# Kernel optimization log

Hardware: AMD Instinct MI355X
Metric: run time of the kernel (lower is better)

Reference implementation:

```python
import jax, jax.numpy as jnp
import numpy as np
from itertools import combinations

# ---- G(3,0,1) projective geometric algebra tables (blade order: grades 0..4, lexicographic) ----

def _build_tables():
    blades = [c for g in range(5) for c in combinations(range(4), g)]
    index = {b: i for i, b in enumerate(blades)}
    def mul(a, b, e0_sq):
        lst = list(a) + list(b)
        sign = 1
        for i in range(len(lst)):
            for j in range(len(lst) - 1 - i):
                if lst[j] > lst[j + 1]:
                    lst[j], lst[j + 1] = lst[j + 1], lst[j]
                    sign = -sign
        out, i = [], 0
        while i < len(lst):
            if i + 1 < len(lst) and lst[i] == lst[i + 1]:
                if lst[i] == 0:
                    sign *= e0_sq  # e0^2 = 0 in PGA geometric product
                i += 2
            else:
                out.append(lst[i]); i += 1
        return tuple(out), sign
    GP = np.zeros((16, 16, 16), np.float32)
    WEDGE = np.zeros((16, 16, 16), np.float32)
    for a in blades:
        for b in blades:
            bl, s = mul(a, b, 0)
            if s != 0:
                GP[index[a], index[b], index[bl]] += s
            if not (set(a) & set(b)):
                bl, s = mul(a, b, 1)
                WEDGE[index[a], index[b], index[bl]] += s
    D = np.zeros((16, 16), np.float32)
    for a in blades:
        c = tuple(sorted(set(range(4)) - set(a)))
        bl, s = mul(a, c, 1)  # e_a ^ e_c = s * e0123
        D[index[c], index[a]] = s
    Dinv = np.linalg.inv(D).astype(np.float32)
    # 9 Pin(3,0,1)-equivariant linear basis maps: 5 grade projections + 4 left-mult by e0
    B = np.zeros((9, 16, 16), np.float32)
    for i, a in enumerate(blades):
        B[len(a), i, i] = 1.0
        if 0 not in a:
            tgt = tuple(sorted((0,) + a))
            B[5 + len(a), index[tgt], i] = 1.0
    inner_idx = np.array([i for i, a in enumerate(blades) if 0 not in a])  # invariant inner product skips e0 blades
    return (jnp.asarray(GP), jnp.asarray(WEDGE), jnp.asarray(D), jnp.asarray(Dinv), jnp.asarray(B), jnp.asarray(inner_idx))

GP_T, WEDGE_T, DUAL, DUAL_INV, BASIS, INNER_IDX = _build_tables()
N_HEADS = 8  # gatr SelfAttentionConfig default


def equi_linear(x, W):
    # x: [..., in_ch, 16], W: [out_ch, in_ch, 9] -> [..., out_ch, 16]
    return jnp.einsum('...ik,oib,bjk->...oj', x, W, BASIS)


def equi_norm(x, eps=1e-6):
    sq = jnp.sum(jnp.take(x, INNER_IDX, axis=-1) ** 2, axis=-1)      # [..., C]
    factor = jnp.mean(sq, axis=-1, keepdims=True)[..., None]          # [..., 1, 1]
    return x * jax.lax.rsqrt(factor + eps)


def geometric_product(x, y):
    return jnp.einsum('...i,...j,ijk->...k', x, y, GP_T)


def equi_join(x, y):
    xd = jnp.einsum('ji,...i->...j', DUAL, x)
    yd = jnp.einsum('ji,...i->...j', DUAL, y)
    w = jnp.einsum('...i,...j,ijk->...k', xd, yd, WEDGE_T)
    return jnp.einsum('ji,...i->...j', DUAL_INV, w)


def attention(x, Wq, Wk, Wv, Wo):
    Bb, N, C, _ = x.shape
    ch = C // N_HEADS
    def split(h):
        return h.reshape(Bb, N, N_HEADS, ch, 16).transpose(0, 2, 1, 3, 4)  # [B,H,N,ch,16]
    q = split(equi_linear(x, Wq))
    k = split(equi_linear(x, Wk))
    v = split(equi_linear(x, Wv))
    qi = jnp.take(q, INNER_IDX, axis=-1)
    ki = jnp.take(k, INNER_IDX, axis=-1)
    logits = jnp.einsum('bhnck,bhmck->bhnm', qi, ki) / np.float32(np.sqrt(8 * ch))
    att = jax.nn.softmax(logits, axis=-1)
    out = jnp.einsum('bhnm,bhmck->bhnck', att, v)
    out = out.transpose(0, 2, 1, 3, 4).reshape(Bb, N, C, 16)
    return equi_linear(out, Wo)


def geo_mlp(x, Wl, Wr, Wm):
    C = x.shape[-2]
    half = C // 2
    left = equi_linear(x, Wl)
    right = equi_linear(x, Wr)
    gp = geometric_product(left[..., :half, :], right[..., :half, :])
    jn = equi_join(left[..., half:, :], right[..., half:, :])
    h = jnp.concatenate([gp, jn], axis=-2)
    h = h * jax.nn.gelu(h[..., 0:1], approximate=False)  # scalar-gated GELU
    return equi_linear(h, Wm)


def embed_point(p):
    # PGA point: homogeneous trivector, e123 coefficient 1
    z = jnp.zeros(p.shape[:-1] + (16,), p.dtype)
    z = z.at[..., 11].set(p[..., 2])
    z = z.at[..., 12].set(-p[..., 1])
    z = z.at[..., 13].set(p[..., 0])
    z = z.at[..., 14].set(1.0)
    return z


def reference(points, W_in, Wq, Wk, Wv, Wo, Wl, Wr, Wm, W_out):
    x = embed_point(points)[..., None, :]   # [B, N, 1, 16]
    x = equi_linear(x, W_in)                # [B, N, C, 16]
    def block(xc, p):
        wq, wk, wv, wo, wl, wr, wm = p
        xc = xc + attention(equi_norm(xc), wq, wk, wv, wo)
        xc = xc + geo_mlp(equi_norm(xc), wl, wr, wm)
        return xc, None
    x, _ = jax.lax.scan(block, x, (Wq, Wk, Wv, Wo, Wl, Wr, Wm))
    out = equi_linear(x, W_out)             # [B, N, 1, 16]
    return jnp.mean(out[..., 0], axis=(1, 2))  # [B]


def setup_inputs():
    key = jax.random.key(0)
    ks = jax.random.split(key, 12)
    B, N, C, L = 1, 2048, 16, 10
    def w(k, o, i):
        return jax.random.normal(k, (o, i, 9), jnp.float32) / np.float32(np.sqrt(9.0 * i))
    def wl(k, o, i):
        return jax.random.normal(k, (L, o, i, 9), jnp.float32) / np.float32(np.sqrt(9.0 * i))
    return {
        'points': jax.random.normal(ks[0], (B, N, 3), jnp.float32),
        'W_in': w(ks[1], C, 1),
        'Wq': wl(ks[2], C, C), 'Wk': wl(ks[3], C, C), 'Wv': wl(ks[4], C, C),
        'Wo': wl(ks[5], C, C), 'Wl': wl(ks[6], C, C), 'Wr': wl(ks[7], C, C),
        'Wm': wl(ks[8], C, C), 'W_out': w(ks[9], 1, C),
    }
```

## Files before the change

### kernel.cpp

```cpp
#include <hip/hip_runtime.h>
#include <hip/hip_bf16.h>
#include <math.h>

#define NTOK 2048

typedef short short8v __attribute__((ext_vector_type(8)));
typedef short short4v __attribute__((ext_vector_type(4)));
typedef float f32x4 __attribute__((ext_vector_type(4)));
typedef unsigned u32x4 __attribute__((ext_vector_type(4)));

__device__ __forceinline__ unsigned short f2bf(float x){
  unsigned u = __float_as_uint(x);
  u += 0x7fff + ((u>>16)&1);
  return (unsigned short)(u>>16);
}
__device__ __forceinline__ unsigned pack_bf2(float a, float b){
  __hip_bfloat162 h = __float22bfloat162_rn(float2{a,b});
  return *reinterpret_cast<unsigned*>(&h);
}

struct GEnt { unsigned char i, j, k; signed char s; };

constexpr int IDX2MASK[16] = {0,1,2,4,8,3,5,9,6,10,12,7,11,13,14,15};
constexpr int MASK2IDX[16] = {0,1,2,5,3,6,8,11,4,7,9,12,10,13,14,15};

constexpr int rsign(int a, int b){
  int cnt=0;
  for(int i=0;i<4;++i) if((b>>i)&1) for(int j=i+1;j<4;++j) if((a>>j)&1) cnt++;
  return (cnt&1)?-1:1;
}

struct GPTab { GEnt e[192]; };
constexpr GPTab make_gp(){
  GPTab t{}; int n=0;
  for(int ia=0; ia<16; ++ia) for(int ib=0; ib<16; ++ib){
    int a=IDX2MASK[ia], b=IDX2MASK[ib];
    if(a&b&1) continue;
    t.e[n].i=(unsigned char)ia; t.e[n].j=(unsigned char)ib;
    t.e[n].k=(unsigned char)MASK2IDX[a^b]; t.e[n].s=(signed char)rsign(a,b);
    ++n;
  }
  return t;
}
static constexpr GPTab GP_TAB = make_gp();

struct JTab { GEnt e[81]; };
constexpr JTab make_join(){
  JTab t{}; int n=0;
  for(int ia=0; ia<16; ++ia) for(int ib=0; ib<16; ++ib){
    int a=IDX2MASK[ia], b=IDX2MASK[ib];
    if((a|b)!=15) continue;
    int ca=(~a)&15, cb=(~b)&15, k=a&b, ck=(~k)&15;
    int s = rsign(a,ca)*rsign(b,cb)*rsign(ca,cb)*rsign(k,ck);
    t.e[n].i=(unsigned char)ia; t.e[n].j=(unsigned char)ib;
    t.e[n].k=(unsigned char)MASK2IDX[k]; t.e[n].s=(signed char)s;
    ++n;
  }
  return t;
}
static constexpr JTab J_TAB = make_join();

constexpr int INNER[8] = {0,2,3,4,8,9,10,14};

__device__ __forceinline__ void apply_gp(float* o, const float* a, const float* b){
#pragma unroll
  for(int n=0;n<192;++n){
    const float s = (float)GP_TAB.e[n].s;
    o[GP_TAB.e[n].k] = fmaf(s*a[GP_TAB.e[n].i], b[GP_TAB.e[n].j], o[GP_TAB.e[n].k]);
  }
}
__device__ __forceinline__ void apply_join(float* o, const float* a, const float* b){
#pragma unroll
  for(int n=0;n<81;++n){
    const float s = (float)J_TAB.e[n].s;
    o[J_TAB.e[n].k] = fmaf(s*a[J_TAB.e[n].i], b[J_TAB.e[n].j], o[J_TAB.e[n].k]);
  }
}

__device__ __forceinline__ void elin_row(float acc[16], const float* xin, const float* w0p){
#pragma unroll
  for(int j=0;j<16;++j) acc[j]=0.0f;
#pragma unroll
  for(int i=0;i<16;++i){
    const float* w = w0p + i*9;
    const float4* xp = (const float4*)(xin + i*16);
    float4 A=xp[0], B=xp[1], Cc=xp[2], D=xp[3];
    float w0=w[0],w1=w[1],w2=w[2],w3=w[3],w4=w[4],w5=w[5],w6=w[6],w7=w[7],w8=w[8];
    acc[0] = fmaf(w0, A.x,  acc[0]);
    acc[1] = fmaf(w1, A.y,  acc[1]);
    acc[2] = fmaf(w1, A.z,  acc[2]);
    acc[3] = fmaf(w1, A.w,  acc[3]);
    acc[4] = fmaf(w1, B.x,  acc[4]);
    acc[5] = fmaf(w2, B.y,  acc[5]);
    acc[6] = fmaf(w2, B.z,  acc[6]);
    acc[7] = fmaf(w2, B.w,  acc[7]);
    acc[8] = fmaf(w2, Cc.x, acc[8]);
    acc[9] = fmaf(w2, Cc.y, acc[9]);
    acc[10]= fmaf(w2, Cc.z, acc[10]);
    acc[11]= fmaf(w3, Cc.w, acc[11]);
    acc[12]= fmaf(w3, D.x,  acc[12]);
    acc[13]= fmaf(w3, D.y,  acc[13]);
    acc[14]= fmaf(w3, D.z,  acc[14]);
    acc[15]= fmaf(w4, D.w,  acc[15]);
    acc[1] = fmaf(w5, A.x,  acc[1]);
    acc[5] = fmaf(w6, A.z,  acc[5]);
    acc[6] = fmaf(w6, A.w,  acc[6]);
    acc[7] = fmaf(w6, B.x,  acc[7]);
    acc[11]= fmaf(w7, Cc.x, acc[11]);
    acc[12]= fmaf(w7, Cc.y, acc[12]);
    acc[13]= fmaf(w7, Cc.z, acc[13]);
    acc[15]= fmaf(w8, D.z,  acc[15]);
  }
}

__device__ __forceinline__ float gelu_exact(float x){
  return 0.5f*x*(1.0f+erff(x*0.70710678118654752f));
}

#define WPAD 145
#define TBS  264
#define TPB  8

template<int MODE>
__global__ __launch_bounds__(128) void token_kernel(
    const float* __restrict__ points, const float* __restrict__ Win,
    const float* __restrict__ Wo, const float* __restrict__ Wl,
    const float* __restrict__ Wr, const float* __restrict__ Wm,
    const float* __restrict__ Wq, const float* __restrict__ Wk,
    const float* __restrict__ Wv, const float* __restrict__ Wout,
    const float* __restrict__ ATT, float* __restrict__ X,
    unsigned short* __restrict__ Qg16, unsigned short* __restrict__ Kg16,
    unsigned short* __restrict__ VgT, float* __restrict__ toksum)
{
  __shared__ float wlds[6*16*WPAD];
  __shared__ float buf[TPB*TBS];
  __shared__ float sred[TPB*16];
  const int tid = threadIdx.x;
  const int t = tid>>4, o = tid&15;
  const int n = blockIdx.x*TPB + t;

  auto stage = [&](float* dst, const float* src){
#pragma unroll
    for(int r=0;r<18;++r){
      int k = tid + r*128;
      dst[(k/144)*WPAD + (k%144)] = src[k];
    }
  };
  if (MODE==0){ stage(wlds+3*16*WPAD, Wq); stage(wlds+4*16*WPAD, Wk); stage(wlds+5*16*WPAD, Wv); }
  if (MODE==1){ stage(wlds+0*16*WPAD, Wl); stage(wlds+1*16*WPAD, Wr); stage(wlds+2*16*WPAD, Wm);
                stage(wlds+3*16*WPAD, Wq); stage(wlds+4*16*WPAD, Wk); stage(wlds+5*16*WPAD, Wv); }
  if (MODE==2){ stage(wlds+0*16*WPAD, Wl); stage(wlds+1*16*WPAD, Wr); stage(wlds+2*16*WPAD, Wm); }

  float* tb = buf + t*TBS;
  float xr[16];

  if (MODE==0){
    float px = points[n*3+0], py = points[n*3+1], pz = points[n*3+2];
    float w3 = Win[o*9+3], w8 = Win[o*9+8];
#pragma unroll
    for(int j=0;j<16;++j) xr[j]=0.0f;
    xr[11]= w3*pz; xr[12]= -w3*py; xr[13]= w3*px; xr[14]= w3; xr[15]= w8;
    float4* xg = (float4*)(X + (size_t)n*256 + o*16);
    xg[0]=make_float4(xr[0],xr[1],xr[2],xr[3]);
    xg[1]=make_float4(xr[4],xr[5],xr[6],xr[7]);
    xg[2]=make_float4(xr[8],xr[9],xr[10],xr[11]);
    xg[3]=make_float4(xr[12],xr[13],xr[14],xr[15]);
  } else {
    const float4* xg = (const float4*)(X + (size_t)n*256 + o*16);
    float4 a=xg[0],b=xg[1],c=xg[2],d=xg[3];
    xr[0]=a.x; xr[1]=a.y; xr[2]=a.z; xr[3]=a.w;
    xr[4]=b.x; xr[5]=b.y; xr[6]=b.z; xr[7]=b.w;
    xr[8]=c.x; xr[9]=c.y; xr[10]=c.z; xr[11]=c.w;
    xr[12]=d.x; xr[13]=d.y; xr[14]=d.z; xr[15]=d.w;
    const float4* ag = (const float4*)(ATT + (size_t)n*256 + o*16);
    float4* bp = (float4*)(tb + o*16);
    bp[0]=ag[0]; bp[1]=ag[1]; bp[2]=ag[2]; bp[3]=ag[3];
    __syncthreads();
    float acc[16];
    elin_row(acc, tb, Wo + o*144);
#pragma unroll
    for(int j=0;j<16;++j) xr[j]+=acc[j];
    float s=0;
#pragma unroll
    for(int z=0;z<8;++z){ float v=xr[INNER[z]]; s=fmaf(v,v,s); }
    sred[tid]=s; __syncthreads();
    float tot=0;
#pragma unroll
    for(int c2=0;c2<16;++c2) tot += sred[t*16+c2];
    float f = 1.0f/sqrtf(tot*(1.0f/16.0f)+1e-6f);
    float4* bp2=(float4*)(tb+o*16);
    bp2[0]=make_float4(xr[0]*f,xr[1]*f,xr[2]*f,xr[3]*f);
    bp2[1]=make_float4(xr[4]*f,xr[5]*f,xr[6]*f,xr[7]*f);
    bp2[2]=make_float4(xr[8]*f,xr[9]*f,xr[10]*f,xr[11]*f);
    bp2[3]=make_float4(xr[12]*f,xr[13]*f,xr[14]*f,xr[15]*f);
    __syncthreads();
    float L[16], R[16];
    elin_row(L, tb, wlds+0*16*WPAD + o*WPAD);
    elin_row(R, tb, wlds+1*16*WPAD + o*WPAD);
    float h[16];
#pragma unroll
    for(int j=0;j<16;++j) h[j]=0.0f;
    if (o<8) apply_gp(h,L,R); else apply_join(h,L,R);
    float gel = gelu_exact(h[0]);
#pragma unroll
    for(int j=0;j<16;++j) h[j]*=gel;
    __syncthreads();
    float4* bp3=(float4*)(tb+o*16);
    bp3[0]=make_float4(h[0],h[1],h[2],h[3]);
    bp3[1]=make_float4(h[4],h[5],h[6],h[7]);
    bp3[2]=make_float4(h[8],h[9],h[10],h[11]);
    bp3[3]=make_float4(h[12],h[13],h[14],h[15]);
    __syncthreads();
    float mm2[16];
    elin_row(mm2, tb, wlds+2*16*WPAD + o*WPAD);
#pragma unroll
    for(int j=0;j<16;++j) xr[j]+=mm2[j];
    if (MODE==1){
      float4* xs = (float4*)(X + (size_t)n*256 + o*16);
      xs[0]=make_float4(xr[0],xr[1],xr[2],xr[3]);
      xs[1]=make_float4(xr[4],xr[5],xr[6],xr[7]);
      xs[2]=make_float4(xr[8],xr[9],xr[10],xr[11]);
      xs[3]=make_float4(xr[12],xr[13],xr[14],xr[15]);
    }
  }

  if (MODE==2){
    sred[tid] = Wout[o*9]*xr[0];
    __syncthreads();
    if (o==0){
      float s2=0;
#pragma unroll
      for(int c2=0;c2<16;++c2) s2+=sred[t*16+c2];
      toksum[n]=s2;
    }
    return;
  }

  {
    float s=0;
#pragma unroll
    for(int z=0;z<8;++z){ float v=xr[INNER[z]]; s=fmaf(v,v,s); }
    sred[tid]=s; __syncthreads();
    float tot=0;
#pragma unroll
    for(int c2=0;c2<16;++c2) tot += sred[t*16+c2];
    float f2 = 1.0f/sqrtf(tot*(1.0f/16.0f)+1e-6f);
    float4* bp4=(float4*)(tb+o*16);
    bp4[0]=make_float4(xr[0]*f2,xr[1]*f2,xr[2]*f2,xr[3]*f2);
    bp4[1]=make_float4(xr[4]*f2,xr[5]*f2,xr[6]*f2,xr[7]*f2);
    bp4[2]=make_float4(xr[8]*f2,xr[9]*f2,xr[10]*f2,xr[11]*f2);
    bp4[3]=make_float4(xr[12]*f2,xr[13]*f2,xr[14]*f2,xr[15]*f2);
    __syncthreads();
    float q_[16],k_[16],v_[16];
    elin_row(q_, tb, wlds+3*16*WPAD+o*WPAD);
    elin_row(k_, tb, wlds+4*16*WPAD+o*WPAD);
    elin_row(v_, tb, wlds+5*16*WPAD+o*WPAD);
    int hh=o>>1, cc=o&1;
    {
      unsigned qw[4], kw[4];
#pragma unroll
      for(int j=0;j<4;++j){
        unsigned short a0=f2bf(q_[INNER[2*j]]*0.25f), a1=f2bf(q_[INNER[2*j+1]]*0.25f);
        unsigned short b0=f2bf(k_[INNER[2*j]]),       b1=f2bf(k_[INNER[2*j+1]]);
        qw[j] = (unsigned)a0 | ((unsigned)a1<<16);
        kw[j] = (unsigned)b0 | ((unsigned)b1<<16);
      }
      size_t rb = ((size_t)hh*NTOK + n)*16 + cc*8;
      *(uint4*)(Qg16 + rb) = make_uint4(qw[0],qw[1],qw[2],qw[3]);
      *(uint4*)(Kg16 + rb) = make_uint4(kw[0],kw[1],kw[2],kw[3]);
    }
    __syncthreads();
    {
      float4* vb = (float4*)(tb + o*16);
      vb[0]=make_float4(v_[0],v_[1],v_[2],v_[3]);
      vb[1]=make_float4(v_[4],v_[5],v_[6],v_[7]);
      vb[2]=make_float4(v_[8],v_[9],v_[10],v_[11]);
      vb[3]=make_float4(v_[12],v_[13],v_[14],v_[15]);
    }
    __syncthreads();
#pragma unroll
    for(int pp=0;pp<2;++pp){
      int p  = tid + pp*128;
      int h2 = p>>5, v2 = p&31;
      int oc = 2*h2 + (v2>>4), c2 = v2&15;
      unsigned vw[4];
#pragma unroll
      for(int j=0;j<4;++j){
        unsigned short e0=f2bf(buf[(2*j  )*TBS + oc*16 + c2]);
        unsigned short e1=f2bf(buf[(2*j+1)*TBS + oc*16 + c2]);
        vw[j]=(unsigned)e0 | ((unsigned)e1<<16);
      }
      *(uint4*)(VgT + ((size_t)(h2*32+v2))*NTOK + (size_t)blockIdx.x*TPB) = make_uint4(vw[0],vw[1],vw[2],vw[3]);
    }
  }
}

__global__ __launch_bounds__(512, 8) void attn_kernel(
    const unsigned short* __restrict__ Qg16, const unsigned short* __restrict__ Kg16,
    const unsigned short* __restrict__ VgT,  float* __restrict__ ATT)
{
  __shared__ float cmb[8*32*17];
  __shared__ float ml[8*16*2];
  const int tid = threadIdx.x;
  const int l   = tid & 63, w = tid >> 6;
  const int h   = blockIdx.x >> 7, qb = blockIdx.x & 127;
  const int l15 = l & 15, lg = l >> 4;

  const short4v z4 = {0,0,0,0};
  short8v qf;
  {
    const short4v* qp = (const short4v*)(Qg16 + ((size_t)(h*NTOK + qb*16 + l15))*16 + lg*4);
    qf = __builtin_shufflevector(*qp, z4, 0,1,2,3,4,5,6,7);
  }

  const int key0 = w*256;
  const size_t vrow = ((size_t)(h*32 + l15))*NTOK;

  float mx = -INFINITY;
#pragma unroll 1
  for(int kc=0; kc<256; kc+=64){
#pragma unroll
    for(int t2=0;t2<4;++t2){
      const short4v* kp = (const short4v*)(Kg16 + ((size_t)(h*NTOK + key0 + kc + t2*16 + l15))*16 + lg*4);
      short8v kf = __builtin_shufflevector(*kp, z4, 0,1,2,3,4,5,6,7);
      f32x4 z = {0,0,0,0};
      f32x4 S = __builtin_amdgcn_mfma_f32_16x16x32_bf16(kf, qf, z, 0,0,0);
      mx = fmaxf(mx, fmaxf(fmaxf(S[0],S[1]), fmaxf(S[2],S[3])));
    }
  }
  mx = fmaxf(mx, __shfl_xor(mx, 16));
  mx = fmaxf(mx, __shfl_xor(mx, 32));
  const float M = mx;

  f32x4 acc0 = {0,0,0,0}, acc1 = {0,0,0,0};
  float ls = 0.0f;
#pragma unroll 1
  for(int kc=0; kc<256; kc+=64){
    f32x4 S[4];
#pragma unroll
    for(int t2=0;t2<4;++t2){
      const short4v* kp = (const short4v*)(Kg16 + ((size_t)(h*NTOK + key0 + kc + t2*16 + l15))*16 + lg*4);
      short8v kf = __builtin_shufflevector(*kp, z4, 0,1,2,3,4,5,6,7);
      f32x4 z = {0,0,0,0};
      S[t2] = __builtin_amdgcn_mfma_f32_16x16x32_bf16(kf, qf, z, 0,0,0);
    }
    float p[4][4];
#pragma unroll
    for(int t2=0;t2<4;++t2)
#pragma unroll
      for(int r=0;r<4;++r){ float pv = __expf(S[t2][r]-M); p[t2][r]=pv; ls += pv; }
    u32x4 paw, paw2;
    paw[0]=pack_bf2(p[0][0],p[0][1]); paw[1]=pack_bf2(p[0][2],p[0][3]);
    paw[2]=pack_bf2(p[1][0],p[1][1]); paw[3]=pack_bf2(p[1][2],p[1][3]);
    paw2[0]=pack_bf2(p[2][0],p[2][1]); paw2[1]=pack_bf2(p[2][2],p[2][3]);
    paw2[2]=pack_bf2(p[3][0],p[3][1]); paw2[3]=pack_bf2(p[3][2],p[3][3]);
    short8v pa  = *reinterpret_cast<short8v*>(&paw);
    short8v pa2 = *reinterpret_cast<short8v*>(&paw2);
    size_t vb = vrow + key0 + kc;
    const short4v* v0a = (const short4v*)(VgT + vb + lg*4);
    const short4v* v0b = (const short4v*)(VgT + vb + 16 + lg*4);
    const short4v* v0c = (const short4v*)(VgT + vb + 32 + lg*4);
    const short4v* v0d = (const short4v*)(VgT + vb + 48 + lg*4);
    short8v vb0  = __builtin_shufflevector(*v0a, *v0b, 0,1,2,3,4,5,6,7);
    short8v vb0b = __builtin_shufflevector(*v0c, *v0d, 0,1,2,3,4,5,6,7);
    size_t vb1s = vb + (size_t)16*NTOK;
    const short4v* v1a = (const short4v*)(VgT + vb1s + lg*4);
    const short4v* v1b = (const short4v*)(VgT + vb1s + 16 + lg*4);
    const short4v* v1c = (const short4v*)(VgT + vb1s + 32 + lg*4);
    const short4v* v1d = (const short4v*)(VgT + vb1s + 48 + lg*4);
    short8v vb1  = __builtin_shufflevector(*v1a, *v1b, 0,1,2,3,4,5,6,7);
    short8v vb1b = __builtin_shufflevector(*v1c, *v1d, 0,1,2,3,4,5,6,7);
    acc0 = __builtin_amdgcn_mfma_f32_16x16x32_bf16(pa,  vb0,  acc0, 0,0,0);
    acc0 = __builtin_amdgcn_mfma_f32_16x16x32_bf16(pa2, vb0b, acc0, 0,0,0);
    acc1 = __builtin_amdgcn_mfma_f32_16x16x32_bf16(pa,  vb1,  acc1, 0,0,0);
    acc1 = __builtin_amdgcn_mfma_f32_16x16x32_bf16(pa2, vb1b, acc1, 0,0,0);
  }
  ls += __shfl_xor(ls, 16);
  ls += __shfl_xor(ls, 32);

  {
    float* cw = cmb + w*544;
#pragma unroll
    for(int r=0;r<4;++r){
      cw[ l15     *17 + lg*4 + r] = acc0[r];
      cw[(l15+16) *17 + lg*4 + r] = acc1[r];
    }
    if (lg == 0){
      ml[(w*16 + l15)*2]   = M;
      ml[(w*16 + l15)*2+1] = ls;
    }
  }
  __syncthreads();
  {
    int q = tid & 15, v = tid >> 4;
    float Mg = -INFINITY;
#pragma unroll
    for(int w2=0; w2<8; ++w2) Mg = fmaxf(Mg, ml[(w2*16+q)*2]);
    float L=0, a=0;
#pragma unroll
    for(int w2=0; w2<8; ++w2){
      float ww = __expf(ml[(w2*16+q)*2] - Mg);
      L = fmaf(ml[(w2*16+q)*2+1], ww, L);
      a = fmaf(cmb[w2*544 + v*17 + q], ww, a);
    }
    int n = qb*16 + q;
    ATT[(size_t)n*256 + (size_t)(2*h + (v>>4))*16 + (v&15)] = a/L;
  }
}

__global__ __launch_bounds__(256) void reduce_kernel(const float* __restrict__ tok, float* __restrict__ out){
  int tid=threadIdx.x;
  float s=0;
  for(int i=tid;i<NTOK;i+=256) s+=tok[i];
#pragma unroll
  for(int off=32;off>0;off>>=1) s += __shfl_down(s,off);
  __shared__ float red[4];
  if((tid&63)==0) red[tid>>6]=s;
  __syncthreads();
  if(tid==0) out[0]=(red[0]+red[1]+red[2]+red[3])*(1.0f/2048.0f);
}

extern "C" void kernel_launch(void* const* d_in, const int* in_sizes, int n_in,
                              void* d_out, int out_size, void* d_ws, size_t ws_size,
                              hipStream_t stream){
  const float* points=(const float*)d_in[0];
  const float* Win=(const float*)d_in[1];
  const float* Wq=(const float*)d_in[2];
  const float* Wk=(const float*)d_in[3];
  const float* Wv=(const float*)d_in[4];
  const float* Wo=(const float*)d_in[5];
  const float* Wl=(const float*)d_in[6];
  const float* Wr=(const float*)d_in[7];
  const float* Wm=(const float*)d_in[8];
  const float* Wout=(const float*)d_in[9];
  float* ws=(float*)d_ws;
  float* X    = ws;
  float* ATT  = ws + 524288;
  unsigned short* Qg16 = (unsigned short*)(ws + 1048576);
  unsigned short* Kg16 = (unsigned short*)(ws + 1179648);
  unsigned short* VgT  = (unsigned short*)(ws + 1310720);
  float* tok  = ws + 1572864;
  float* out=(float*)d_out;

  token_kernel<0><<<256,128,0,stream>>>(points,Win,nullptr,nullptr,nullptr,nullptr,
                                        Wq,Wk,Wv,nullptr,nullptr,X,Qg16,Kg16,VgT,nullptr);
  for(int l=0;l<10;++l){
    attn_kernel<<<1024,512,0,stream>>>(Qg16,Kg16,VgT,ATT);
    if(l<9){
      token_kernel<1><<<256,128,0,stream>>>(nullptr,nullptr,
          Wo+l*2304,Wl+l*2304,Wr+l*2304,Wm+l*2304,
          Wq+(l+1)*2304,Wk+(l+1)*2304,Wv+(l+1)*2304,nullptr,
          ATT,X,Qg16,Kg16,VgT,nullptr);
    } else {
      token_kernel<2><<<256,128,0,stream>>>(nullptr,nullptr,
          Wo+l*2304,Wl+l*2304,Wr+l*2304,Wm+l*2304,
          nullptr,nullptr,nullptr,Wout,
          ATT,X,nullptr,nullptr,nullptr,tok);
    }
  }
  reduce_kernel<<<1,256,0,stream>>>(tok,out);
}
```

Before: 677.4 us.

## Split token kernel per-token work across a wavefront with shuffle reductions

Each token is now handled by one 64-lane wavefront instead of 16 threads. The 16 input channels of every equivariant linear layer are split into four partial sums, which are combined with cross-lane shuffles. Weights are re-laid out in LDS as padded 12-float rows so they can be read with vector loads, and Wo is also staged in LDS. Block barriers are replaced by in-wave LDS waits, and the norm and output reductions use shuffles instead of shared memory. The intent is more parallelism and fewer block-wide barriers in the serial token stage. In exchange, each block now re-stages the QKV weights a second time, and lanes that do not write stay idle.

```diff
diff --git a/kernel.cpp b/kernel.cpp
--- a/kernel.cpp
+++ b/kernel.cpp
@@ -77,15 +77,25 @@
   }
 }
 
-__device__ __forceinline__ void elin_row(float acc[16], const float* xin, const float* w0p){
+__device__ __forceinline__ float gelu_exact(float x){
+  return 0.5f*x*(1.0f+erff(x*0.70710678118654752f));
+}
+
+#define TBS 264
+
+__device__ __forceinline__ void elin_part(float acc[16], const float* xin, const float* wslot, int o, int s){
 #pragma unroll
   for(int j=0;j<16;++j) acc[j]=0.0f;
 #pragma unroll
-  for(int i=0;i<16;++i){
-    const float* w = w0p + i*9;
+  for(int ii=0; ii<4; ++ii){
+    int i = s*4 + ii;
+    const float* w = wslot + (i*16 + o)*12;
+    float4 wA = *(const float4*)(w);
+    float4 wB = *(const float4*)(w+4);
+    float w8 = w[8];
     const float4* xp = (const float4*)(xin + i*16);
     float4 A=xp[0], B=xp[1], Cc=xp[2], D=xp[3];
-    float w0=w[0],w1=w[1],w2=w[2],w3=w[3],w4=w[4],w5=w[5],w6=w[6],w7=w[7],w8=w[8];
+    float w0=wA.x,w1=wA.y,w2=wA.z,w3=wA.w,w4=wB.x,w5=wB.y,w6=wB.z,w7=wB.w;
     acc[0] = fmaf(w0, A.x,  acc[0]);
     acc[1] = fmaf(w1, A.y,  acc[1]);
     acc[2] = fmaf(w1, A.z,  acc[2]);
@@ -113,16 +123,27 @@
   }
 }
 
-__device__ __forceinline__ float gelu_exact(float x){
-  return 0.5f*x*(1.0f+erff(x*0.70710678118654752f));
-}
-
-#define WPAD 145
-#define TBS  264
-#define TPB  8
+__device__ __forceinline__ void combine16(float a[16]){
+#pragma unroll
+  for(int k=0;k<16;++k){
+    a[k] += __shfl_xor(a[k],16);
+    a[k] += __shfl_xor(a[k],32);
+  }
+}
+
+__device__ __forceinline__ float normfac(const float xr[16]){
+  float part=0;
+#pragma unroll
+  for(int z=0;z<8;++z){ float v=xr[INNER[z]]; part=fmaf(v,v,part); }
+  part += __shfl_xor(part,1); part += __shfl_xor(part,2);
+  part += __shfl_xor(part,4); part += __shfl_xor(part,8);
+  return 1.0f/sqrtf(part*(1.0f/16.0f)+1e-6f);
+}
+
+#define LDSWAIT asm volatile("s_waitcnt lgkmcnt(0)" ::: "memory"); __builtin_amdgcn_sched_barrier(0);
 
 template<int MODE>
-__global__ __launch_bounds__(128) void token_kernel(
+__global__ __launch_bounds__(256) void token_kernel(
     const float* __restrict__ points, const float* __restrict__ Win,
     const float* __restrict__ Wo, const float* __restrict__ Wl,
     const float* __restrict__ Wr, const float* __restrict__ Wm,
@@ -132,39 +153,41 @@
     unsigned short* __restrict__ Qg16, unsigned short* __restrict__ Kg16,
     unsigned short* __restrict__ VgT, float* __restrict__ toksum)
 {
-  __shared__ float wlds[6*16*WPAD];
-  __shared__ float buf[TPB*TBS];
-  __shared__ float sred[TPB*16];
+  __shared__ float wlds[4*3072];
+  __shared__ float buf[4*TBS];
   const int tid = threadIdx.x;
-  const int t = tid>>4, o = tid&15;
-  const int n = blockIdx.x*TPB + t;
+  const int t = tid>>6, lane = tid&63;
+  const int o = lane&15, s = lane>>4;
+  const int n = blockIdx.x*4 + t;
+  float* tb = buf + t*TBS;
 
   auto stage = [&](float* dst, const float* src){
 #pragma unroll
-    for(int r=0;r<18;++r){
-      int k = tid + r*128;
-      dst[(k/144)*WPAD + (k%144)] = src[k];
+    for(int r=0;r<9;++r){
+      int k = tid + r*256;
+      int oo = k/144, rm = k%144, ii = rm/9, jj = rm%9;
+      dst[(ii*16+oo)*12 + jj] = src[k];
     }
   };
-  if (MODE==0){ stage(wlds+3*16*WPAD, Wq); stage(wlds+4*16*WPAD, Wk); stage(wlds+5*16*WPAD, Wv); }
-  if (MODE==1){ stage(wlds+0*16*WPAD, Wl); stage(wlds+1*16*WPAD, Wr); stage(wlds+2*16*WPAD, Wm);
-                stage(wlds+3*16*WPAD, Wq); stage(wlds+4*16*WPAD, Wk); stage(wlds+5*16*WPAD, Wv); }
-  if (MODE==2){ stage(wlds+0*16*WPAD, Wl); stage(wlds+1*16*WPAD, Wr); stage(wlds+2*16*WPAD, Wm); }
-
-  float* tb = buf + t*TBS;
+  if (MODE==0){ stage(wlds+0*3072, Wq); stage(wlds+1*3072, Wk); stage(wlds+2*3072, Wv); }
+  else        { stage(wlds+0*3072, Wo); stage(wlds+1*3072, Wl); stage(wlds+2*3072, Wr); stage(wlds+3*3072, Wm); }
+  __syncthreads();
+
   float xr[16];
 
   if (MODE==0){
     float px = points[n*3+0], py = points[n*3+1], pz = points[n*3+2];
-    float w3 = Win[o*9+3], w8 = Win[o*9+8];
+    float w3 = Win[o*9+3], w8e = Win[o*9+8];
 #pragma unroll
     for(int j=0;j<16;++j) xr[j]=0.0f;
-    xr[11]= w3*pz; xr[12]= -w3*py; xr[13]= w3*px; xr[14]= w3; xr[15]= w8;
-    float4* xg = (float4*)(X + (size_t)n*256 + o*16);
-    xg[0]=make_float4(xr[0],xr[1],xr[2],xr[3]);
-    xg[1]=make_float4(xr[4],xr[5],xr[6],xr[7]);
-    xg[2]=make_float4(xr[8],xr[9],xr[10],xr[11]);
-    xg[3]=make_float4(xr[12],xr[13],xr[14],xr[15]);
+    xr[11]= w3*pz; xr[12]= -w3*py; xr[13]= w3*px; xr[14]= w3; xr[15]= w8e;
+    if (s==0){
+      float4* xg = (float4*)(X + (size_t)n*256 + o*16);
+      xg[0]=make_float4(xr[0],xr[1],xr[2],xr[3]);
+      xg[1]=make_float4(xr[4],xr[5],xr[6],xr[7]);
+      xg[2]=make_float4(xr[8],xr[9],xr[10],xr[11]);
+      xg[3]=make_float4(xr[12],xr[13],xr[14],xr[15]);
+    }
   } else {
     const float4* xg = (const float4*)(X + (size_t)n*256 + o*16);
     float4 a=xg[0],b=xg[1],c=xg[2],d=xg[3];
@@ -172,31 +195,29 @@
     xr[4]=b.x; xr[5]=b.y; xr[6]=b.z; xr[7]=b.w;
     xr[8]=c.x; xr[9]=c.y; xr[10]=c.z; xr[11]=c.w;
     xr[12]=d.x; xr[13]=d.y; xr[14]=d.z; xr[15]=d.w;
-    const float4* ag = (const float4*)(ATT + (size_t)n*256 + o*16);
-    float4* bp = (float4*)(tb + o*16);
-    bp[0]=ag[0]; bp[1]=ag[1]; bp[2]=ag[2]; bp[3]=ag[3];
-    __syncthreads();
+    if (s==0){
+      const float4* ag = (const float4*)(ATT + (size_t)n*256 + o*16);
+      float4* bp = (float4*)(tb + o*16);
+      bp[0]=ag[0]; bp[1]=ag[1]; bp[2]=ag[2]; bp[3]=ag[3];
+    }
+    LDSWAIT
     float acc[16];
-    elin_row(acc, tb, Wo + o*144);
+    elin_part(acc, tb, wlds+0*3072, o, s);
+    combine16(acc);
 #pragma unroll
     for(int j=0;j<16;++j) xr[j]+=acc[j];
-    float s=0;
-#pragma unroll
-    for(int z=0;z<8;++z){ float v=xr[INNER[z]]; s=fmaf(v,v,s); }
-    sred[tid]=s; __syncthreads();
-    float tot=0;
-#pragma unroll
-    for(int c2=0;c2<16;++c2) tot += sred[t*16+c2];
-    float f = 1.0f/sqrtf(tot*(1.0f/16.0f)+1e-6f);
-    float4* bp2=(float4*)(tb+o*16);
-    bp2[0]=make_float4(xr[0]*f,xr[1]*f,xr[2]*f,xr[3]*f);
-    bp2[1]=make_float4(xr[4]*f,xr[5]*f,xr[6]*f,xr[7]*f);
-    bp2[2]=make_float4(xr[8]*f,xr[9]*f,xr[10]*f,xr[11]*f);
-    bp2[3]=make_float4(xr[12]*f,xr[13]*f,xr[14]*f,xr[15]*f);
-    __syncthreads();
+    float f = normfac(xr);
+    if (s==0){
+      float4* bp=(float4*)(tb+o*16);
+      bp[0]=make_float4(xr[0]*f,xr[1]*f,xr[2]*f,xr[3]*f);
+      bp[1]=make_float4(xr[4]*f,xr[5]*f,xr[6]*f,xr[7]*f);
+      bp[2]=make_float4(xr[8]*f,xr[9]*f,xr[10]*f,xr[11]*f);
+      bp[3]=make_float4(xr[12]*f,xr[13]*f,xr[14]*f,xr[15]*f);
+    }
+    LDSWAIT
     float L[16], R[16];
-    elin_row(L, tb, wlds+0*16*WPAD + o*WPAD);
-    elin_row(R, tb, wlds+1*16*WPAD + o*WPAD);
+    elin_part(L, tb, wlds+1*3072, o, s); combine16(L);
+    elin_part(R, tb, wlds+2*3072, o, s); combine16(R);
     float h[16];
 #pragma unroll
     for(int j=0;j<16;++j) h[j]=0.0f;
@@ -204,18 +225,19 @@
     float gel = gelu_exact(h[0]);
 #pragma unroll
     for(int j=0;j<16;++j) h[j]*=gel;
-    __syncthreads();
-    float4* bp3=(float4*)(tb+o*16);
-    bp3[0]=make_float4(h[0],h[1],h[2],h[3]);
-    bp3[1]=make_float4(h[4],h[5],h[6],h[7]);
-    bp3[2]=make_float4(h[8],h[9],h[10],h[11]);
-    bp3[3]=make_float4(h[12],h[13],h[14],h[15]);
-    __syncthreads();
-    float mm2[16];
-    elin_row(mm2, tb, wlds+2*16*WPAD + o*WPAD);
-#pragma unroll
-    for(int j=0;j<16;++j) xr[j]+=mm2[j];
-    if (MODE==1){
+    if (s==0){
+      float4* bp=(float4*)(tb+o*16);
+      bp[0]=make_float4(h[0],h[1],h[2],h[3]);
+      bp[1]=make_float4(h[4],h[5],h[6],h[7]);
+      bp[2]=make_float4(h[8],h[9],h[10],h[11]);
+      bp[3]=make_float4(h[12],h[13],h[14],h[15]);
+    }
+    LDSWAIT
+    float mm[16];
+    elin_part(mm, tb, wlds+3*3072, o, s); combine16(mm);
+#pragma unroll
+    for(int j=0;j<16;++j) xr[j]+=mm[j];
+    if (MODE==1 && s==0){
       float4* xs = (float4*)(X + (size_t)n*256 + o*16);
       xs[0]=make_float4(xr[0],xr[1],xr[2],xr[3]);
       xs[1]=make_float4(xr[4],xr[5],xr[6],xr[7]);
@@ -225,73 +247,67 @@
   }
 
   if (MODE==2){
-    sred[tid] = Wout[o*9]*xr[0];
+    float val = Wout[o*9]*xr[0];
+    val += __shfl_xor(val,1); val += __shfl_xor(val,2);
+    val += __shfl_xor(val,4); val += __shfl_xor(val,8);
+    if (lane==0) toksum[n]=val;
+    return;
+  }
+
+  if (MODE==1){
     __syncthreads();
-    if (o==0){
-      float s2=0;
-#pragma unroll
-      for(int c2=0;c2<16;++c2) s2+=sred[t*16+c2];
-      toksum[n]=s2;
-    }
-    return;
+    stage(wlds+0*3072, Wq); stage(wlds+1*3072, Wk); stage(wlds+2*3072, Wv);
+    __syncthreads();
   }
 
   {
-    float s=0;
-#pragma unroll
-    for(int z=0;z<8;++z){ float v=xr[INNER[z]]; s=fmaf(v,v,s); }
-    sred[tid]=s; __syncthreads();
-    float tot=0;
-#pragma unroll
-    for(int c2=0;c2<16;++c2) tot += sred[t*16+c2];
-    float f2 = 1.0f/sqrtf(tot*(1.0f/16.0f)+1e-6f);
-    float4* bp4=(float4*)(tb+o*16);
-    bp4[0]=make_float4(xr[0]*f2,xr[1]*f2,xr[2]*f2,xr[3]*f2);
-    bp4[1]=make_float4(xr[4]*f2,xr[5]*f2,xr[6]*f2,xr[7]*f2);
-    bp4[2]=make_float4(xr[8]*f2,xr[9]*f2,xr[10]*f2,xr[11]*f2);
-    bp4[3]=make_float4(xr[12]*f2,xr[13]*f2,xr[14]*f2,xr[15]*f2);
-    __syncthreads();
+    float f2 = normfac(xr);
+    if (s==0){
+      float4* bp=(float4*)(tb+o*16);
+      bp[0]=make_float4(xr[0]*f2,xr[1]*f2,xr[2]*f2,xr[3]*f2);
+      bp[1]=make_float4(xr[4]*f2,xr[5]*f2,xr[6]*f2,xr[7]*f2);
+      bp[2]=make_float4(xr[8]*f2,xr[9]*f2,xr[10]*f2,xr[11]*f2);
+      bp[3]=make_float4(xr[12]*f2,xr[13]*f2,xr[14]*f2,xr[15]*f2);
+    }
+    LDSWAIT
     float q_[16],k_[16],v_[16];
-    elin_row(q_, tb, wlds+3*16*WPAD+o*WPAD);
-    elin_row(k_, tb, wlds+4*16*WPAD+o*WPAD);
-    elin_row(v_, tb, wlds+5*16*WPAD+o*WPAD);
+    elin_part(q_, tb, wlds+0*3072, o, s); combine16(q_);
+    elin_part(k_, tb, wlds+1*3072, o, s); combine16(k_);
+    elin_part(v_, tb, wlds+2*3072, o, s); combine16(v_);
     int hh=o>>1, cc=o&1;
-    {
-      unsigned qw[4], kw[4];
-#pragma unroll
-      for(int j=0;j<4;++j){
-        unsigned short a0=f2bf(q_[INNER[2*j]]*0.25f), a1=f2bf(q_[INNER[2*j+1]]*0.25f);
-        unsigned short b0=f2bf(k_[INNER[2*j]]),       b1=f2bf(k_[INNER[2*j+1]]);
-        qw[j] = (unsigned)a0 | ((unsigned)a1<<16);
-        kw[j] = (unsigned)b0 | ((unsigned)b1<<16);
-      }
-      size_t rb = ((size_t)hh*NTOK + n)*16 + cc*8;
+    size_t rb = ((size_t)hh*NTOK + n)*16 + cc*8;
+    if (s==0){
+      unsigned qw[4];
+#pragma unroll
+      for(int j=0;j<4;++j) qw[j] = pack_bf2(q_[INNER[2*j]]*0.25f, q_[INNER[2*j+1]]*0.25f);
       *(uint4*)(Qg16 + rb) = make_uint4(qw[0],qw[1],qw[2],qw[3]);
+    } else if (s==1){
+      unsigned kw[4];
+#pragma unroll
+      for(int j=0;j<4;++j) kw[j] = pack_bf2(k_[INNER[2*j]], k_[INNER[2*j+1]]);
       *(uint4*)(Kg16 + rb) = make_uint4(kw[0],kw[1],kw[2],kw[3]);
     }
-    __syncthreads();
-    {
-      float4* vb = (float4*)(tb + o*16);
-      vb[0]=make_float4(v_[0],v_[1],v_[2],v_[3]);
-      vb[1]=make_float4(v_[4],v_[5],v_[6],v_[7]);
-      vb[2]=make_float4(v_[8],v_[9],v_[10],v_[11]);
-      vb[3]=make_float4(v_[12],v_[13],v_[14],v_[15]);
-    }
-    __syncthreads();
-#pragma unroll
-    for(int pp=0;pp<2;++pp){
-      int p  = tid + pp*128;
-      int h2 = p>>5, v2 = p&31;
-      int oc = 2*h2 + (v2>>4), c2 = v2&15;
-      unsigned vw[4];
-#pragma unroll
-      for(int j=0;j<4;++j){
-        unsigned short e0=f2bf(buf[(2*j  )*TBS + oc*16 + c2]);
-        unsigned short e1=f2bf(buf[(2*j+1)*TBS + oc*16 + c2]);
-        vw[j]=(unsigned)e0 | ((unsigned)e1<<16);
-      }
-      *(uint4*)(VgT + ((size_t)(h2*32+v2))*NTOK + (size_t)blockIdx.x*TPB) = make_uint4(vw[0],vw[1],vw[2],vw[3]);
-    }
+    if (s==0){
+      float4* bp=(float4*)(tb+o*16);
+      bp[0]=make_float4(v_[0],v_[1],v_[2],v_[3]);
+      bp[1]=make_float4(v_[4],v_[5],v_[6],v_[7]);
+      bp[2]=make_float4(v_[8],v_[9],v_[10],v_[11]);
+      bp[3]=make_float4(v_[12],v_[13],v_[14],v_[15]);
+    }
+  }
+  __syncthreads();
+  {
+    int row = tid;
+    int h2 = row>>5, v2 = row&31;
+    int oc = 2*h2 + (v2>>4), c2 = v2&15;
+    float v0 = buf[0*TBS + oc*16 + c2];
+    float v1 = buf[1*TBS + oc*16 + c2];
+    float v2f= buf[2*TBS + oc*16 + c2];
+    float v3f= buf[3*TBS + oc*16 + c2];
+    uint2 out;
+    out.x = pack_bf2(v0,v1);
+    out.y = pack_bf2(v2f,v3f);
+    *(uint2*)(VgT + (size_t)row*NTOK + blockIdx.x*4) = out;
   }
 }
 
@@ -442,17 +458,17 @@
   float* tok  = ws + 1572864;
   float* out=(float*)d_out;
 
-  token_kernel<0><<<256,128,0,stream>>>(points,Win,nullptr,nullptr,nullptr,nullptr,
+  token_kernel<0><<<512,256,0,stream>>>(points,Win,nullptr,nullptr,nullptr,nullptr,
                                         Wq,Wk,Wv,nullptr,nullptr,X,Qg16,Kg16,VgT,nullptr);
   for(int l=0;l<10;++l){
     attn_kernel<<<1024,512,0,stream>>>(Qg16,Kg16,VgT,ATT);
     if(l<9){
-      token_kernel<1><<<256,128,0,stream>>>(nullptr,nullptr,
+      token_kernel<1><<<512,256,0,stream>>>(nullptr,nullptr,
           Wo+l*2304,Wl+l*2304,Wr+l*2304,Wm+l*2304,
           Wq+(l+1)*2304,Wk+(l+1)*2304,Wv+(l+1)*2304,nullptr,
           ATT,X,Qg16,Kg16,VgT,nullptr);
     } else {
-      token_kernel<2><<<256,128,0,stream>>>(nullptr,nullptr,
+      token_kernel<2><<<512,256,0,stream>>>(nullptr,nullptr,
           Wo+l*2304,Wl+l*2304,Wr+l*2304,Wm+l*2304,
           nullptr,nullptr,nullptr,Wout,
           ATT,X,nullptr,nullptr,nullptr,tok);
```

New measurement: 646.7 us. -4.5%, faster.
